# Kernel optimization log

Hardware: AMD Instinct MI355X
Metric: run time of the kernel (lower is better)

## Reference

```python
import jax, jax.numpy as jnp
import numpy as np

B, N, D_IN, D_OUT, H, W = 2, 2048, 1024, 1024, 16, 64
DH = D_OUT // H


def setup_inputs() -> dict:
    key = jax.random.key(0)
    ks = jax.random.split(key, 6)
    x = jax.random.normal(ks[0], (B, N, D_IN), dtype=jnp.float32)
    s_in = 1.0 / np.sqrt(D_IN)
    s_out = 1.0 / np.sqrt(D_OUT)
    wq = jax.random.normal(ks[1], (D_IN, D_OUT), dtype=jnp.float32) * s_in
    wk = jax.random.normal(ks[2], (D_IN, D_OUT), dtype=jnp.float32) * s_in
    wv = jax.random.normal(ks[3], (D_IN, D_OUT), dtype=jnp.float32) * s_in
    wo = jax.random.normal(ks[4], (D_OUT, D_OUT), dtype=jnp.float32) * s_out
    # sparse global tokens: every 256th token is global
    global_attention = (jnp.arange(N)[None, :] % 256 == 0) & jnp.ones((B, 1), bool)
    return {"x": x, "wq": wq, "wk": wk, "wv": wv, "wo": wo,
            "global_attention": global_attention}


def _mask(global_attention):
    # True = masked out. Causal local window + global rows/cols unmasked.
    i = jnp.arange(N)[:, None]
    j = jnp.arange(N)[None, :]
    allowed = (i - j < W) & (i >= j)          # causal sliding window
    local_mask = ~allowed                      # [N, N], True = masked
    g = global_attention                       # [B, N] bool
    # global token j clears row j and column j of the mask
    global_clear = g[:, :, None] | g[:, None, :]   # [B, N, N]
    return local_mask[None, :, :] & ~global_clear  # [B, N, N]


def reference(x, wq, wk, wv, wo, global_attention):
    b, n, _ = x.shape
    q = (x @ wq).reshape(b, n, H, DH).transpose(0, 2, 1, 3)  # [b,h,n,dh]
    k = (x @ wk).reshape(b, n, H, DH).transpose(0, 2, 1, 3)
    v = (x @ wv).reshape(b, n, H, DH).transpose(0, 2, 1, 3)
    scores = jnp.einsum('bhqd,bhkd->bhqk', q, k) / jnp.sqrt(jnp.float32(DH))
    mask = _mask(global_attention)[:, None, :, :]            # [b,1,n,n]
    scores = jnp.where(mask, -jnp.inf, scores)
    attn = jax.nn.softmax(scores, axis=-1)
    ctx = jnp.einsum('bhqk,bhkd->bqhd', attn, v).reshape(b, n, D_OUT)
    return ctx @ wo
```

## Files before the change

kernel.cpp:

```cpp
#include <hip/hip_runtime.h>


using u16 = unsigned short;
using u32 = unsigned int;

typedef __attribute__((ext_vector_type(8))) short bf16x8;
typedef __attribute__((ext_vector_type(4))) float f32x4;

__device__ __forceinline__ float b2f(u16 s) {
  union { u32 u; float f; } x; x.u = ((u32)s) << 16; return x.f;
}
__device__ __forceinline__ u16 f2b(float f) {
  union { float f; u32 u; } x; x.f = f;
  u32 r = (x.u + 0x7fffu + ((x.u >> 16) & 1u)) >> 16;
  return (u16)r;
}

__global__ __launch_bounds__(256) void k_pre(const float* __restrict__ x,
                                             u16* __restrict__ xb,
                                             const float* __restrict__ wq,
                                             const float* __restrict__ wk,
                                             const float* __restrict__ wv,
                                             const float* __restrict__ wo,
                                             u16* __restrict__ wqkvT,
                                             u16* __restrict__ woT) {
  __shared__ float tile[64][65];
  const int bid = blockIdx.x;
  if (bid < 2048) {
    int idx = (bid * 256 + threadIdx.x) * 8;
    float4 a = *(const float4*)(x + idx);
    float4 b = *(const float4*)(x + idx + 4);
    uint4 o;
    o.x = (u32)f2b(a.x) | ((u32)f2b(a.y) << 16);
    o.y = (u32)f2b(a.z) | ((u32)f2b(a.w) << 16);
    o.z = (u32)f2b(b.x) | ((u32)f2b(b.y) << 16);
    o.w = (u32)f2b(b.z) | ((u32)f2b(b.w) << 16);
    *(uint4*)(xb + idx) = o;
  } else {
    const int id = bid - 2048;
    const int z = id >> 8, xy = id & 255;
    const float* src = (z == 0) ? wq : (z == 1) ? wk : (z == 2) ? wv : wo;
    u16* dst = (z < 3) ? (wqkvT + ((size_t)z << 20)) : woT;
    const int n0 = (xy & 15) * 64, k0 = (xy >> 4) * 64;
    const int tx = threadIdx.x & 63, ty = threadIdx.x >> 6;
    #pragma unroll
    for (int r = 0; r < 64; r += 4)
      tile[r + ty][tx] = src[(size_t)(k0 + r + ty) * 1024 + n0 + tx];
    __syncthreads();
    #pragma unroll
    for (int r = 0; r < 64; r += 4)
      dst[(size_t)(n0 + r + ty) * 1024 + k0 + tx] = f2b(tile[tx][r + ty]);
  }
}

__device__ __forceinline__ void gload16(const u16* g, u16* l) {
  __builtin_amdgcn_global_load_lds((const __attribute__((address_space(1))) void*)g,
                                   (__attribute__((address_space(3))) void*)l, 16, 0, 0);
}

__global__ __launch_bounds__(512, 2) void k_qkv256(const u16* __restrict__ A,
                                                   const u16* __restrict__ Bt,
                                                   u16* __restrict__ C) {
  __shared__ __attribute__((aligned(16))) u16 lds[57344];
  const int K = 1024, N = 3072, NT = 16;
  const int t = threadIdx.x;
  const int wid = t >> 6, lane = t & 63;
  const int l4 = lane >> 4, l16 = lane & 15;
  const int qr = wid >> 1, qc = wid & 1;
  const int d = blockIdx.y * gridDim.x + blockIdx.x;
  const int qq = (gridDim.x * gridDim.y) >> 3;
  const int tau = (d & 7) * qq + (d >> 3);
  const int bn = tau % gridDim.x, bm = tau / gridDim.x;
  const u16* Ab = A + (size_t)bm * 256 * K;
  const u16* Bb = Bt + (size_t)bn * 192 * K;
  const int rowbase = wid * 8 + (lane >> 3);
  const int qcg = rowbase >> 5, rrb = rowbase & 31;
  const int scc = ((lane & 7) ^ ((lane >> 3) & 7)) << 3;
  const int rsw = (l16 & 7);
  f32x4 acc[3][4][2] = {};
  bf16x8 af[4][2], bf[2][2];

  #define STG_A(BUF, KT, H)                                                        \
    { u16* lb = lds + (BUF) * 16384 + (H) * 8192 + (wid << 9);                     \
      _Pragma("unroll")                                                            \
      for (int i = 0; i < 2; ++i)                                                  \
        gload16(Ab + (size_t)((H) * 128 + i * 64 + rowbase) * K + (KT) * 64 + scc, \
                lb + i * 4096); }

  #define STG_B1(BUF, KT, I)                                                       \
    { u16* lb = lds + 32768 + (BUF) * 12288 + (I) * 4096 + (wid << 9);             \
      gload16(Bb + (size_t)(qcg * 96 + (I) * 32 + rrb) * K + (KT) * 64 + scc, lb); }

  #define LOAD_A(AS)                                                               \
    { _Pragma("unroll")                                                            \
      for (int m = 0; m < 4; ++m) {                                                \
        const int ro = qr * 64 + m * 16 + l16;                                     \
        _Pragma("unroll")                                                          \
        for (int ks = 0; ks < 2; ++ks)                                             \
          af[m][ks] = *(const bf16x8*)&(AS)[ro * 64 + (((ks * 4 + l4) ^ rsw) << 3)]; \
      } }

  #define LOAD_B(BS, NH)                                                           \
    { _Pragma("unroll")                                                            \
      for (int n = 0; n < 2; ++n) {                                                \
        const int po = (NH) * 64 + qc * 32 + n * 16 + l16;                         \
        _Pragma("unroll")                                                          \
        for (int ks = 0; ks < 2; ++ks)                                             \
          bf[n][ks] = *(const bf16x8*)&(BS)[po * 64 + (((ks * 4 + l4) ^ rsw) << 3)]; \
      } }

  #define QUAD(NH)                                                                 \
    { __builtin_amdgcn_s_setprio(1);                                               \
      _Pragma("unroll")                                                            \
      for (int m = 0; m < 4; ++m)                                                  \
        _Pragma("unroll")                                                          \
        for (int n = 0; n < 2; ++n) {                                              \
          f32x4 c = acc[NH][m][n];                                                 \
          c = __builtin_amdgcn_mfma_f32_16x16x32_bf16(af[m][0], bf[n][0], c, 0, 0, 0); \
          c = __builtin_amdgcn_mfma_f32_16x16x32_bf16(af[m][1], bf[n][1], c, 0, 0, 0); \
          acc[NH][m][n] = c;                                                       \
        }                                                                          \
      __builtin_amdgcn_s_setprio(0); }

  STG_A(0, 0, 0); STG_A(0, 0, 1);
  STG_B1(0, 0, 0); STG_B1(0, 0, 1); STG_B1(0, 0, 2);
  STG_A(1, 1, 0); STG_A(1, 1, 1);
  STG_B1(1, 1, 0);
  asm volatile("s_waitcnt vmcnt(5)" ::: "memory");
  __builtin_amdgcn_s_barrier();

  for (int tt = 0; tt < NT; ++tt) {
    const int beta = tt & 1;
    const u16* As = lds + beta * 16384;
    const u16* Bs = lds + 32768 + beta * 12288;
    LOAD_A(As);
    LOAD_B(Bs, 0);
    if (tt + 1 < NT) STG_B1(beta ^ 1, tt + 1, 1);
    __builtin_amdgcn_s_barrier();
    QUAD(0);
    __builtin_amdgcn_s_barrier();
    LOAD_B(Bs, 1);
    if (tt + 1 < NT) STG_B1(beta ^ 1, tt + 1, 2);
    __builtin_amdgcn_s_barrier();
    QUAD(1);
    __builtin_amdgcn_s_barrier();
    LOAD_B(Bs, 2);
    if (tt + 2 < NT) {
      STG_A(beta, tt + 2, 0);
      STG_A(beta, tt + 2, 1);
      STG_B1(beta, tt + 2, 0);
    }
    __builtin_amdgcn_s_barrier();
    QUAD(2);
    if (tt + 2 < NT)      asm volatile("s_waitcnt vmcnt(5)" ::: "memory");
    else if (tt + 1 < NT) asm volatile("s_waitcnt vmcnt(0)" ::: "memory");
    __builtin_amdgcn_s_barrier();
  }
  #undef STG_A
  #undef STG_B1
  #undef LOAD_A
  #undef LOAD_B
  #undef QUAD

  #pragma unroll
  for (int nh = 0; nh < 3; ++nh)
    #pragma unroll
    for (int m = 0; m < 4; ++m) {
      const int row0 = bm * 256 + qr * 64 + m * 16 + l4 * 4;
      #pragma unroll
      for (int n = 0; n < 2; ++n) {
        const int col = bn * 192 + qc * 96 + nh * 32 + n * 16 + l16;
        #pragma unroll
        for (int r = 0; r < 4; ++r)
          C[(size_t)(row0 + r) * N + col] = f2b(acc[nh][m][n][r]);
      }
    }
}

template<int F32OUT, int GRED>
__global__ __launch_bounds__(256, 2) void k_gemm64(const u16* __restrict__ A,
                                                   const u16* __restrict__ Bt,
                                                   void* __restrict__ C, int N, int K,
                                                   const float* __restrict__ gpart,
                                                   u16* __restrict__ ctxw) {
  __shared__ u16 lds[3][6144];
  const int t = threadIdx.x;
  const int wid = t >> 6, lane = t & 63;
  const int l4 = lane >> 4, l16 = lane & 15;
  const int wr = wid >> 1, wc = wid & 1;
  const int d = blockIdx.y * gridDim.x + blockIdx.x;
  const int qq = (gridDim.x * gridDim.y) >> 3;
  const int tau = (d & 7) * qq + (d >> 3);
  const int bn = tau % gridDim.x, bm = tau / gridDim.x;
  const u16* Ab = A + (size_t)bm * 64 * K;
  const u16* Bb = Bt + (size_t)bn * 128 * K;
  const int srow0 = t >> 2;
  const int scol = (((t & 3) ^ ((t >> 3) & 3)) << 3);
  const int sdst = wid << 9;
  const int sl8 = ((l4 ^ ((l16 >> 1) & 3)) << 3);
  const int NT = K >> 5;
  f32x4 acc[2][4] = {};

  if (GRED && (bm & 3) == 0) {
    const int bb = bm >> 5;
    const int irow = (bm & 31) * 64;
    const int row8 = (bm & 31) >> 2;
    const int h = t >> 4;
    const int d0 = (t & 15) * 4;
    const float* g0 = gpart + ((size_t)(bb * 16 + h) * 32) * 520;
    float o0 = 0.f, o1 = 0.f, o2 = 0.f, o3 = 0.f, ls = 0.f;
    for (int q = 0; q < 32; ++q) {
      const float4 v = *(const float4*)(g0 + q * 520 + row8 * 64 + d0);
      o0 += v.x; o1 += v.y; o2 += v.z; o3 += v.w;
      ls += g0[q * 520 + 512 + row8];
    }
    const float inv = 1.f / ls;
    u16* cw = ctxw + ((size_t)(bb * 2048 + irow)) * 1024 + h * 64 + d0;
    cw[0] = f2b(o0 * inv); cw[1] = f2b(o1 * inv);
    cw[2] = f2b(o2 * inv); cw[3] = f2b(o3 * inv);
    __syncthreads();
  }

  #pragma unroll
  for (int pt = 0; pt < 2; ++pt) {
    gload16(Ab + (size_t)srow0 * K + (pt << 5) + scol, &lds[pt][sdst]);
    #pragma unroll
    for (int c = 0; c < 2; ++c)
      gload16(Bb + (size_t)(c * 64 + srow0) * K + (pt << 5) + scol,
              &lds[pt][2048 + c * 2048 + sdst]);
  }

  int cur = 0, nxt2 = 2;
  for (int tt = 0; tt < NT; ++tt) {
    if (tt + 1 < NT) asm volatile("s_waitcnt vmcnt(3)" ::: "memory");
    else             asm volatile("s_waitcnt vmcnt(0)" ::: "memory");
    __builtin_amdgcn_s_barrier();
    if (tt + 2 < NT) {
      const int k0 = (tt + 2) << 5;
      u16* dst = &lds[nxt2][0];
      gload16(Ab + (size_t)srow0 * K + k0 + scol, dst + sdst);
      #pragma unroll
      for (int c = 0; c < 2; ++c)
        gload16(Bb + (size_t)(c * 64 + srow0) * K + k0 + scol, dst + 2048 + c * 2048 + sdst);
    }
    const u16* As = lds[cur];
    const u16* Bs = lds[cur] + 2048;
    bf16x8 af[2], bf[4];
    #pragma unroll
    for (int m = 0; m < 2; ++m)
      af[m] = *(const bf16x8*)&As[(wr * 32 + m * 16 + l16) * 32 + sl8];
    #pragma unroll
    for (int n = 0; n < 4; ++n)
      bf[n] = *(const bf16x8*)&Bs[(wc * 64 + n * 16 + l16) * 32 + sl8];
    __builtin_amdgcn_s_setprio(1);
    #pragma unroll
    for (int m = 0; m < 2; ++m)
      #pragma unroll
      for (int n = 0; n < 4; ++n)
        acc[m][n] = __builtin_amdgcn_mfma_f32_16x16x32_bf16(af[m], bf[n], acc[m][n], 0, 0, 0);
    __builtin_amdgcn_s_setprio(0);
    cur = (cur == 2) ? 0 : cur + 1;
    nxt2 = (nxt2 == 2) ? 0 : nxt2 + 1;
  }

  #pragma unroll
  for (int m = 0; m < 2; ++m) {
    const int row0 = bm * 64 + wr * 32 + m * 16 + l4 * 4;
    #pragma unroll
    for (int n = 0; n < 4; ++n) {
      const int col = bn * 128 + wc * 64 + n * 16 + l16;
      #pragma unroll
      for (int r = 0; r < 4; ++r) {
        if (F32OUT) ((float*)C)[(size_t)(row0 + r) * N + col] = acc[m][n][r];
        else        ((u16*)C)[(size_t)(row0 + r) * N + col] = f2b(acc[m][n][r]);
      }
    }
  }
}

__global__ __launch_bounds__(256) void k_attn_tile(const u16* __restrict__ qkv,
                                                   u16* __restrict__ ctx,
                                                   float* __restrict__ gpart) {
  __shared__ u16 buf[26880];
  __shared__ u16 Qgs[16 * 72];
  __shared__ u16 Pgs[16 * 72];
  __shared__ float lred[4][16];
  u16* Qs = buf;
  u16* Ks = buf + 4608;
  u16* Vt = buf + 16128;
  u16* Ps = buf;

  const int t = threadIdx.x, wid = t >> 6, lane = t & 63;
  const int l4 = lane >> 4, l16 = lane & 15;
  const int qt = blockIdx.x, h = blockIdx.y, b = blockIdx.z;
  const int q0 = qt * 64;
  const int kbase = q0 - 64;
  const size_t base = (size_t)b * 2048 * 3072;
  const u16* Qg = qkv + base + h * 64;
  const u16* Kg = qkv + base + 1024 + h * 64;
  const u16* Vg = qkv + base + 2048 + h * 64;

  for (int s = t; s < 512; s += 256) {
    int r = s >> 3, c = (s & 7) * 8;
    *(uint4*)&Qs[r * 72 + c] = *(const uint4*)&Qg[(size_t)(q0 + r) * 3072 + c];
  }
  if (t < 128) {
    int r = t >> 3, c = (t & 7) * 8;
    if (r < 8) {
      *(uint4*)&Qgs[r * 72 + c] = *(const uint4*)&Qg[(size_t)(r * 256) * 3072 + c];
    } else {
      uint4 z = {0, 0, 0, 0};
      *(uint4*)&Qgs[r * 72 + c] = z;
    }
  }
  for (int s = t; s < 1088; s += 256) {
    int r = s >> 3, c = (s & 7) * 8;
    int j = (r < 128) ? max(kbase + r, 0) : (r - 128) * 256;
    *(uint4*)&Ks[r * 72 + c] = *(const uint4*)&Kg[(size_t)j * 3072 + c];
  }
  for (int s = t; s < 1088; s += 256) {
    int r = s >> 3, c = (s & 7) * 8;
    int j = (r < 128) ? max(kbase + r, 0) : (r - 128) * 256;
    uint4 v = *(const uint4*)&Vg[(size_t)j * 3072 + c];
    const u16* pv = (const u16*)&v;
    const int ch = r >> 3;
    #pragma unroll
    for (int e8 = 0; e8 < 8; ++e8) {
      const int d = c + e8;
      const int kd = ((d >> 3) ^ d) & 7;
      const int chs = (ch < 16) ? (ch ^ kd) : ch;
      Vt[d * 168 + chs * 8 + (r & 7)] = pv[e8];
    }
  }
  for (int z = t; z < 64 * 24; z += 256) {
    int d = z / 24, j = 136 + z % 24;
    Vt[d * 168 + j] = 0;
  }
  __syncthreads();

  f32x4 sa[10] = {};
  #pragma unroll
  for (int ks = 0; ks < 2; ++ks) {
    bf16x8 qa = *(const bf16x8*)&Qs[(wid * 16 + l16) * 72 + ks * 32 + l4 * 8];
    #pragma unroll
    for (int n = 0; n < 10; ++n) {
      bf16x8 kb = *(const bf16x8*)&Ks[(n * 16 + l16) * 72 + ks * 32 + l4 * 8];
      sa[n] = __builtin_amdgcn_mfma_f32_16x16x32_bf16(qa, kb, sa[n], 0, 0, 0);
    }
  }

  f32x4 sg = {};
  #pragma unroll
  for (int ks = 0; ks < 2; ++ks) {
    bf16x8 qa = *(const bf16x8*)&Qgs[l16 * 72 + ks * 32 + l4 * 8];
    bf16x8 kb = *(const bf16x8*)&Ks[(64 + wid * 16 + l16) * 72 + ks * 32 + l4 * 8];
    sg = __builtin_amdgcn_mfma_f32_16x16x32_bf16(qa, kb, sg, 0, 0, 0);
  }
  #pragma unroll
  for (int r = 0; r < 4; ++r) {
    float p = __expf(sg[r] * 0.125f);
    sg[r] = p;
    #pragma unroll
    for (int o = 1; o < 16; o <<= 1) p += __shfl_xor(p, o);
    if (l16 == 0) lred[wid][l4 * 4 + r] = p;
  }
  #pragma unroll
  for (int r = 0; r < 4; ++r)
    Pgs[(l4 * 4 + r) * 72 + wid * 16 + l16] = f2b(sg[r]);

  const int qi0 = wid * 16 + l4 * 4;
  #pragma unroll
  for (int n = 0; n < 10; ++n) {
    const int jc = n * 16 + l16;
    #pragma unroll
    for (int r = 0; r < 4; ++r) {
      const int qi = qi0 + r;
      bool allowed;
      if (n < 8) {
        const int kr = kbase + jc;
        allowed = (jc > qi) && (jc <= qi + 64) && (kr >= 0) && ((kr & 255) != 0);
      } else {
        allowed = (jc < 136);
      }
      sa[n][r] = allowed ? sa[n][r] * 0.125f : -1e30f;
    }
  }

  float m[4], l[4];
  #pragma unroll
  for (int r = 0; r < 4; ++r) {
    float mx = sa[0][r];
    #pragma unroll
    for (int n = 1; n < 10; ++n) mx = fmaxf(mx, sa[n][r]);
    #pragma unroll
    for (int o = 1; o < 16; o <<= 1) mx = fmaxf(mx, __shfl_xor(mx, o));
    m[r] = mx;
    l[r] = 0.f;
  }
  #pragma unroll
  for (int n = 0; n < 10; ++n)
    #pragma unroll
    for (int r = 0; r < 4; ++r) {
      float p = __expf(sa[n][r] - m[r]);
      sa[n][r] = p;
      l[r] += p;
    }
  #pragma unroll
  for (int r = 0; r < 4; ++r)
    #pragma unroll
    for (int o = 1; o < 16; o <<= 1) l[r] += __shfl_xor(l[r], o);

  __syncthreads();

  u16* Pw = Ps + wid * (16 * 168);
  #pragma unroll
  for (int n = 0; n < 10; ++n)
    #pragma unroll
    for (int r = 0; r < 4; ++r)
      Pw[(l4 * 4 + r) * 168 + n * 16 + l16] = f2b(sa[n][r]);
  __syncthreads();

  f32x4 o[4] = {};
  #pragma unroll
  for (int ks = 0; ks < 5; ++ks) {
    bf16x8 pa = *(const bf16x8*)&Pw[l16 * 168 + ks * 32 + l4 * 8];
    #pragma unroll
    for (int dt = 0; dt < 4; ++dt) {
      const int dvo = dt * 16 + l16;
      const int kdo = ((dvo >> 3) ^ dvo) & 7;
      const int ch = ks * 4 + l4;
      const int chs = (ch < 16) ? (ch ^ kdo) : ch;
      bf16x8 vb = *(const bf16x8*)&Vt[dvo * 168 + chs * 8];
      o[dt] = __builtin_amdgcn_mfma_f32_16x16x32_bf16(pa, vb, o[dt], 0, 0, 0);
    }
  }

  f32x4 og = {};
  {
    const int dV = wid * 16 + l16;
    const int kdg = ((dV >> 3) ^ dV) & 7;
    #pragma unroll
    for (int ks = 0; ks < 2; ++ks) {
      bf16x8 pa = *(const bf16x8*)&Pgs[l16 * 72 + ks * 32 + l4 * 8];
      const int chs = (8 + ks * 4 + l4) ^ kdg;
      bf16x8 vb = *(const bf16x8*)&Vt[dV * 168 + chs * 8];
      og = __builtin_amdgcn_mfma_f32_16x16x32_bf16(pa, vb, og, 0, 0, 0);
    }
  }
  float* gp = gpart + ((size_t)(b * 16 + h) * 32 + qt) * 520;
  #pragma unroll
  for (int r = 0; r < 4; ++r) {
    int row = l4 * 4 + r;
    if (row < 8) gp[row * 64 + wid * 16 + l16] = og[r];
  }
  if (t < 8) gp[512 + t] = lred[0][t] + lred[1][t] + lred[2][t] + lred[3][t];

  #pragma unroll
  for (int r = 0; r < 4; ++r) {
    const int q = q0 + qi0 + r;
    if ((q & 255) == 0) continue;
    const float inv = 1.0f / l[r];
    #pragma unroll
    for (int dt = 0; dt < 4; ++dt)
      ctx[(size_t)(b * 2048 + q) * 1024 + h * 64 + dt * 16 + l16] = f2b(o[dt][r] * inv);
  }
}

extern "C" void kernel_launch(void* const* d_in, const int* in_sizes, int n_in,
                              void* d_out, int out_size, void* d_ws, size_t ws_size,
                              hipStream_t stream) {
  (void)in_sizes; (void)n_in; (void)out_size; (void)ws_size;
  const float* x  = (const float*)d_in[0];
  const float* wq = (const float*)d_in[1];
  const float* wk = (const float*)d_in[2];
  const float* wv = (const float*)d_in[3];
  const float* wo = (const float*)d_in[4];
  char* ws = (char*)d_ws;
  u16* xb    = (u16*)(ws);
  u16* qkv   = (u16*)(ws + (8u  << 20));
  u16* ctx   = (u16*)(ws + (32u << 20));
  u16* wqkvT = (u16*)(ws + (40u << 20));
  u16* woT   = (u16*)(ws + (46u << 20));
  float* gpart = (float*)(ws);

  k_pre<<<3072, 256, 0, stream>>>(x, xb, wq, wk, wv, wo, wqkvT, woT);
  k_qkv256<<<dim3(16, 16), 512, 0, stream>>>(xb, wqkvT, qkv);
  k_attn_tile<<<dim3(32, 16, 2), 256, 0, stream>>>(qkv, ctx, gpart);
  k_gemm64<1, 1><<<dim3(8, 64), 256, 0, stream>>>(ctx, woT, d_out, 1024, 1024, gpart, ctx);
}
```

Measured before the change: 82.94 us.

## Replace output GEMM with 128x128-tile, 512-thread kernel using BK=64 double buffering

The output projection GEMM moves from 64x128 tiles with 256 threads and a triple-buffered BK=32 pipeline to 128x128 tiles with 512 threads (8 waves) and a double-buffered BK=64 pipeline with an XOR-swizzled LDS layout. The fused global-token reduction now runs on half the threads of every other row block. Larger tiles raise data reuse per LDS load and halve the iteration count. The grid shrinks from 512 to 256 blocks, which may leave CUs underused on a 256-CU part and needs more LDS per block.

```diff
diff --git a/kernel.cpp b/kernel.cpp
--- a/kernel.cpp
+++ b/kernel.cpp
@@ -177,105 +177,124 @@
     }
 }
 
-template<int F32OUT, int GRED>
-__global__ __launch_bounds__(256, 2) void k_gemm64(const u16* __restrict__ A,
-                                                   const u16* __restrict__ Bt,
-                                                   void* __restrict__ C, int N, int K,
-                                                   const float* __restrict__ gpart,
-                                                   u16* __restrict__ ctxw) {
-  __shared__ u16 lds[3][6144];
+__global__ __launch_bounds__(512, 2) void k_out(const u16* __restrict__ A,
+                                                const u16* __restrict__ Bt,
+                                                float* __restrict__ C,
+                                                const float* __restrict__ gpart,
+                                                u16* __restrict__ ctxw) {
+  __shared__ __attribute__((aligned(16))) u16 lds[32768];
+  const int K = 1024, N = 1024, NT = 16;
   const int t = threadIdx.x;
   const int wid = t >> 6, lane = t & 63;
   const int l4 = lane >> 4, l16 = lane & 15;
-  const int wr = wid >> 1, wc = wid & 1;
+  const int qr = wid >> 2, qc = wid & 3;
   const int d = blockIdx.y * gridDim.x + blockIdx.x;
   const int qq = (gridDim.x * gridDim.y) >> 3;
   const int tau = (d & 7) * qq + (d >> 3);
   const int bn = tau % gridDim.x, bm = tau / gridDim.x;
-  const u16* Ab = A + (size_t)bm * 64 * K;
+  const u16* Ab = A + (size_t)bm * 128 * K;
   const u16* Bb = Bt + (size_t)bn * 128 * K;
-  const int srow0 = t >> 2;
-  const int scol = (((t & 3) ^ ((t >> 3) & 3)) << 3);
-  const int sdst = wid << 9;
-  const int sl8 = ((l4 ^ ((l16 >> 1) & 3)) << 3);
-  const int NT = K >> 5;
+  const int rowbase = wid * 8 + (lane >> 3);
+  const int qcg = rowbase >> 4, rrb = rowbase & 15;
+  const int scc = ((lane & 7) ^ ((lane >> 3) & 7)) << 3;
+  const int rsw = (l16 & 7);
   f32x4 acc[2][4] = {};
-
-  if (GRED && (bm & 3) == 0) {
-    const int bb = bm >> 5;
-    const int irow = (bm & 31) * 64;
-    const int row8 = (bm & 31) >> 2;
-    const int h = t >> 4;
-    const int d0 = (t & 15) * 4;
-    const float* g0 = gpart + ((size_t)(bb * 16 + h) * 32) * 520;
-    float o0 = 0.f, o1 = 0.f, o2 = 0.f, o3 = 0.f, ls = 0.f;
-    for (int q = 0; q < 32; ++q) {
-      const float4 v = *(const float4*)(g0 + q * 520 + row8 * 64 + d0);
-      o0 += v.x; o1 += v.y; o2 += v.z; o3 += v.w;
-      ls += g0[q * 520 + 512 + row8];
-    }
-    const float inv = 1.f / ls;
-    u16* cw = ctxw + ((size_t)(bb * 2048 + irow)) * 1024 + h * 64 + d0;
-    cw[0] = f2b(o0 * inv); cw[1] = f2b(o1 * inv);
-    cw[2] = f2b(o2 * inv); cw[3] = f2b(o3 * inv);
+  bf16x8 af[4][2], bf[2][2];
+
+  if ((bm & 1) == 0) {
+    if (t < 256) {
+      const int bb = bm >> 4;
+      const int irow = (bm & 15) * 128;
+      const int row8 = (bm & 15) >> 1;
+      const int h = t >> 4;
+      const int d0 = (t & 15) * 4;
+      const float* g0 = gpart + ((size_t)(bb * 16 + h) * 32) * 520;
+      float o0 = 0.f, o1 = 0.f, o2 = 0.f, o3 = 0.f, ls = 0.f;
+      for (int q = 0; q < 32; ++q) {
+        const float4 v = *(const float4*)(g0 + q * 520 + row8 * 64 + d0);
+        o0 += v.x; o1 += v.y; o2 += v.z; o3 += v.w;
+        ls += g0[q * 520 + 512 + row8];
+      }
+      const float inv = 1.f / ls;
+      u16* cw = ctxw + ((size_t)(bb * 2048 + irow)) * 1024 + h * 64 + d0;
+      cw[0] = f2b(o0 * inv); cw[1] = f2b(o1 * inv);
+      cw[2] = f2b(o2 * inv); cw[3] = f2b(o3 * inv);
+    }
     __syncthreads();
   }
 
-  #pragma unroll
-  for (int pt = 0; pt < 2; ++pt) {
-    gload16(Ab + (size_t)srow0 * K + (pt << 5) + scol, &lds[pt][sdst]);
-    #pragma unroll
-    for (int c = 0; c < 2; ++c)
-      gload16(Bb + (size_t)(c * 64 + srow0) * K + (pt << 5) + scol,
-              &lds[pt][2048 + c * 2048 + sdst]);
-  }
-
-  int cur = 0, nxt2 = 2;
+  #define OSTG_A(BUF, KT)                                                          \
+    { u16* lb = lds + (BUF) * 8192 + (wid << 9);                                   \
+      _Pragma("unroll")                                                            \
+      for (int i = 0; i < 2; ++i)                                                  \
+        gload16(Ab + (size_t)(i * 64 + rowbase) * K + (KT) * 64 + scc,             \
+                lb + i * 4096); }
+
+  #define OSTG_B(BUF, KT)                                                          \
+    { u16* lb = lds + 16384 + (BUF) * 8192 + (wid << 9);                           \
+      _Pragma("unroll")                                                            \
+      for (int nf = 0; nf < 2; ++nf)                                               \
+        gload16(Bb + (size_t)(qcg * 32 + nf * 16 + rrb) * K + (KT) * 64 + scc,     \
+                lb + nf * 4096); }
+
+  #define OLOAD()                                                                  \
+    { _Pragma("unroll")                                                            \
+      for (int m = 0; m < 4; ++m) {                                                \
+        const int ro = qr * 64 + m * 16 + l16;                                     \
+        _Pragma("unroll")                                                          \
+        for (int ks = 0; ks < 2; ++ks)                                             \
+          af[m][ks] = *(const bf16x8*)&As[ro * 64 + (((ks * 4 + l4) ^ rsw) << 3)]; \
+      }                                                                            \
+      _Pragma("unroll")                                                            \
+      for (int nf = 0; nf < 2; ++nf) {                                             \
+        const int po = nf * 64 + qc * 16 + l16;                                    \
+        _Pragma("unroll")                                                          \
+        for (int ks = 0; ks < 2; ++ks)                                             \
+          bf[nf][ks] = *(const bf16x8*)&Bs[po * 64 + (((ks * 4 + l4) ^ rsw) << 3)]; \
+      } }
+
+  OSTG_A(0, 0); OSTG_B(0, 0);
+  OSTG_A(1, 1); OSTG_B(1, 1);
+  asm volatile("s_waitcnt vmcnt(4)" ::: "memory");
+  __builtin_amdgcn_s_barrier();
+
   for (int tt = 0; tt < NT; ++tt) {
-    if (tt + 1 < NT) asm volatile("s_waitcnt vmcnt(3)" ::: "memory");
-    else             asm volatile("s_waitcnt vmcnt(0)" ::: "memory");
-    __builtin_amdgcn_s_barrier();
-    if (tt + 2 < NT) {
-      const int k0 = (tt + 2) << 5;
-      u16* dst = &lds[nxt2][0];
-      gload16(Ab + (size_t)srow0 * K + k0 + scol, dst + sdst);
+    const int beta = tt & 1;
+    const u16* As = lds + beta * 8192;
+    const u16* Bs = lds + 16384 + beta * 8192;
+    OLOAD();
+    asm volatile("s_waitcnt lgkmcnt(0)" ::: "memory");
+    __builtin_amdgcn_s_barrier();
+    if (tt + 2 < NT) { OSTG_A(beta, tt + 2); OSTG_B(beta, tt + 2); }
+    __builtin_amdgcn_s_setprio(1);
+    #pragma unroll
+    for (int nf = 0; nf < 2; ++nf)
       #pragma unroll
-      for (int c = 0; c < 2; ++c)
-        gload16(Bb + (size_t)(c * 64 + srow0) * K + k0 + scol, dst + 2048 + c * 2048 + sdst);
-    }
-    const u16* As = lds[cur];
-    const u16* Bs = lds[cur] + 2048;
-    bf16x8 af[2], bf[4];
-    #pragma unroll
-    for (int m = 0; m < 2; ++m)
-      af[m] = *(const bf16x8*)&As[(wr * 32 + m * 16 + l16) * 32 + sl8];
-    #pragma unroll
-    for (int n = 0; n < 4; ++n)
-      bf[n] = *(const bf16x8*)&Bs[(wc * 64 + n * 16 + l16) * 32 + sl8];
-    __builtin_amdgcn_s_setprio(1);
-    #pragma unroll
-    for (int m = 0; m < 2; ++m)
+      for (int m = 0; m < 4; ++m) {
+        f32x4 c = acc[nf][m];
+        c = __builtin_amdgcn_mfma_f32_16x16x32_bf16(af[m][0], bf[nf][0], c, 0, 0, 0);
+        c = __builtin_amdgcn_mfma_f32_16x16x32_bf16(af[m][1], bf[nf][1], c, 0, 0, 0);
+        acc[nf][m] = c;
+      }
+    __builtin_amdgcn_s_setprio(0);
+    if (tt + 2 < NT)      asm volatile("s_waitcnt vmcnt(4)" ::: "memory");
+    else if (tt + 1 < NT) asm volatile("s_waitcnt vmcnt(0)" ::: "memory");
+    __builtin_amdgcn_s_barrier();
+  }
+  #undef OSTG_A
+  #undef OSTG_B
+  #undef OLOAD
+
+  #pragma unroll
+  for (int nf = 0; nf < 2; ++nf)
+    #pragma unroll
+    for (int m = 0; m < 4; ++m) {
+      const int row0 = bm * 128 + qr * 64 + m * 16 + l4 * 4;
+      const int col = bn * 128 + qc * 32 + nf * 16 + l16;
       #pragma unroll
-      for (int n = 0; n < 4; ++n)
-        acc[m][n] = __builtin_amdgcn_mfma_f32_16x16x32_bf16(af[m], bf[n], acc[m][n], 0, 0, 0);
-    __builtin_amdgcn_s_setprio(0);
-    cur = (cur == 2) ? 0 : cur + 1;
-    nxt2 = (nxt2 == 2) ? 0 : nxt2 + 1;
-  }
-
-  #pragma unroll
-  for (int m = 0; m < 2; ++m) {
-    const int row0 = bm * 64 + wr * 32 + m * 16 + l4 * 4;
-    #pragma unroll
-    for (int n = 0; n < 4; ++n) {
-      const int col = bn * 128 + wc * 64 + n * 16 + l16;
-      #pragma unroll
-      for (int r = 0; r < 4; ++r) {
-        if (F32OUT) ((float*)C)[(size_t)(row0 + r) * N + col] = acc[m][n][r];
-        else        ((u16*)C)[(size_t)(row0 + r) * N + col] = f2b(acc[m][n][r]);
-      }
-    }
-  }
+      for (int r = 0; r < 4; ++r)
+        C[(size_t)(row0 + r) * N + col] = acc[nf][m][r];
+    }
 }
 
 __global__ __launch_bounds__(256) void k_attn_tile(const u16* __restrict__ qkv,
@@ -486,5 +505,5 @@
   k_pre<<<3072, 256, 0, stream>>>(x, xb, wq, wk, wv, wo, wqkvT, woT);
   k_qkv256<<<dim3(16, 16), 512, 0, stream>>>(xb, wqkvT, qkv);
   k_attn_tile<<<dim3(32, 16, 2), 256, 0, stream>>>(qkv, ctx, gpart);
-  k_gemm64<1, 1><<<dim3(8, 64), 256, 0, stream>>>(ctx, woT, d_out, 1024, 1024, gpart, ctx);
-}
+  k_out<<<dim3(8, 32), 512, 0, stream>>>(ctx, woT, (float*)d_out, gpart, ctx);
+}
```

Result: faster. 79.94 us, median of 2 (-3.6%).
